# Performance work log

Hardware: AMD Instinct MI355X
Metric: run time of the kernel (lower is better)

## Reference

```python
import jax, jax.numpy as jnp
import numpy as np

DIM = 1024
HEADS = 16
HEAD_DIM = DIM // HEADS
B, S = 4, 2048


def setup_inputs() -> dict:
    key = jax.random.key(0)
    ks = jax.random.split(key, 10)
    std = 1.0 / np.sqrt(DIM)
    def lin(k):
        kw, kb = jax.random.split(k)
        W = jax.random.uniform(kw, (DIM, DIM), jnp.float32, -std, std)
        b = jax.random.uniform(kb, (DIM,), jnp.float32, -std, std)
        return W, b
    Wq, bq = lin(ks[0])
    Wk, bk = lin(ks[1])
    Wv, bv = lin(ks[2])
    Wo, bo = lin(ks[3])
    q = jax.random.normal(ks[4], (B, S, DIM), jnp.float32)
    mask = jnp.ones((B, S), dtype=bool)
    return {"q": q, "mask": mask, "Wq": Wq, "bq": bq, "Wk": Wk, "bk": bk,
            "Wv": Wv, "bv": bv, "Wo": Wo, "bo": bo}


def reference(q, mask, Wq, bq, Wk, bk, Wv, bv, Wo, bo):
    # self-attention: k = v = q
    Bsz, Sq, D = q.shape
    scale = HEAD_DIM ** -0.5
    qh = (q @ Wq.T + bq).reshape(Bsz, Sq, HEADS, HEAD_DIM)
    kh = (q @ Wk.T + bk).reshape(Bsz, Sq, HEADS, HEAD_DIM)
    vh = (q @ Wv.T + bv).reshape(Bsz, Sq, HEADS, HEAD_DIM)
    # scores: [B, H, Sq, Sk]
    scores = jnp.einsum('bqhd,bkhd->bhqk', qh, kh) * scale
    neg_inf = jnp.finfo(scores.dtype).min
    # padding mask (batch, seq) -> broadcast over heads and query dim
    scores = jnp.where(mask[:, None, None, :], scores, neg_inf)
    # causal mask
    causal = jnp.triu(jnp.ones((Sq, Sq), dtype=bool), k=1)
    scores = jnp.where(causal[None, None], neg_inf, scores)
    attn = jax.nn.softmax(scores, axis=-1)
    out = jnp.einsum('bhqk,bkhd->bqhd', attn, vh).reshape(Bsz, Sq, D)
    return out @ Wo.T + bo
```

## Files before the change

### kernel.cpp

```cpp
#include <hip/hip_runtime.h>
#include <stdint.h>

#define DIM   1024
#define HEADS 16
#define HD    64
#define BATCH 4
#define SEQ   2048
#define MTOT  (BATCH*SEQ)

typedef __attribute__((ext_vector_type(8))) short bf16x8;
typedef __attribute__((ext_vector_type(4))) float f32x4;

__device__ __forceinline__ unsigned short f2bf(float x) {
    unsigned int u = __float_as_uint(x);
    unsigned int r = (u + 0x7fffu + ((u >> 16) & 1u)) >> 16;
    return (unsigned short)r;
}

__device__ __forceinline__ unsigned int pkbf(float lo, float hi) {
    return __builtin_amdgcn_perm(__float_as_uint(hi) + 0x8000u,
                                 __float_as_uint(lo) + 0x8000u, 0x07060302u);
}
__device__ __forceinline__ unsigned int pktr(float lo, float hi) {
    return __builtin_amdgcn_perm(__float_as_uint(hi),
                                 __float_as_uint(lo), 0x07060302u);
}

__device__ __forceinline__ void gload_lds16(const void* g, void* l) {
    typedef __attribute__((address_space(1))) const unsigned int gbl_uint;
    typedef __attribute__((address_space(3))) unsigned int lds_uint;
    __builtin_amdgcn_global_load_lds(
        reinterpret_cast<gbl_uint*>(reinterpret_cast<uintptr_t>(g)),
        reinterpret_cast<lds_uint*>((unsigned int)reinterpret_cast<uintptr_t>(l)),
        16, 0, 0);
}

__global__ __launch_bounds__(256)
void cast_all(const float* __restrict__ q,
              const float* __restrict__ w0, const float* __restrict__ w1,
              const float* __restrict__ w2, const float* __restrict__ w3,
              unsigned short* __restrict__ qb, unsigned short* __restrict__ wb)
{
    size_t e = ((size_t)blockIdx.x * 256 + threadIdx.x) * 4;
    const float* src; unsigned short* dst; size_t off;
    if (e < (size_t)MTOT * DIM) { src = q; dst = qb; off = e; }
    else {
        size_t we = e - (size_t)MTOT * DIM;
        int wi = (int)(we >> 20);
        off = we & 1048575u;
        src = wi == 0 ? w0 : wi == 1 ? w1 : wi == 2 ? w2 : w3;
        dst = wb + (size_t)wi * 1048576;
    }
    float4 v = *(const float4*)(src + off);
    uint2 r; r.x = pkbf(v.x, v.y); r.y = pkbf(v.z, v.w);
    *(uint2*)(dst + off) = r;
}

template<bool OUT_F32>
__global__ __launch_bounds__(256)
void gemm_mfma(const unsigned short* __restrict__ X,
               const unsigned short* __restrict__ W0, const float* __restrict__ b0, void* __restrict__ O0,
               const unsigned short* __restrict__ W1, const float* __restrict__ b1, void* __restrict__ O1,
               const unsigned short* __restrict__ W2, const float* __restrict__ b2, void* __restrict__ O2,
               float scale0, int vt2)
{
    const unsigned short* W; const float* bias; void* Out;
    if (blockIdx.z == 0)      { W = W0; bias = b0; Out = O0; }
    else if (blockIdx.z == 1) { W = W1; bias = b1; Out = O1; }
    else                      { W = W2; bias = b2; Out = O2; }

    __shared__ unsigned short As[128 * 32];
    __shared__ unsigned short Bs[128 * 32];

    const int t    = threadIdx.x;
    const int wave = t >> 6;
    const int lane = t & 63;
    const int quad = lane >> 4;
    const int l16  = lane & 15;
    const int wm   = wave >> 1;
    const int wn   = wave & 1;
    const int m0   = blockIdx.y * 128;
    const int n0   = blockIdx.x * 128;

    const int srow = lane >> 2;
    const int skof = (lane & 3) * 8;

    f32x4 acc[4][4];
    #pragma unroll
    for (int i = 0; i < 4; ++i)
        #pragma unroll
        for (int j = 0; j < 4; ++j) acc[i][j] = (f32x4){0.f,0.f,0.f,0.f};

    for (int k0 = 0; k0 < 1024; k0 += 32) {
        __syncthreads();
        #pragma unroll
        for (int s = 0; s < 2; ++s) {
            const int ch = wave + s * 4;
            const int row = ch * 16 + srow;
            gload_lds16(X + (size_t)(m0 + row) * 1024 + k0 + skof, &As[ch * 512]);
            gload_lds16(W + (size_t)(n0 + row) * 1024 + k0 + skof, &Bs[ch * 512]);
        }
        __syncthreads();

        bf16x8 af[4], bfr[4];
        #pragma unroll
        for (int i = 0; i < 4; ++i)
            af[i] = *(const bf16x8*)&As[(wm * 64 + i * 16 + l16) * 32 + quad * 8];
        #pragma unroll
        for (int j = 0; j < 4; ++j)
            bfr[j] = *(const bf16x8*)&Bs[(wn * 64 + j * 16 + l16) * 32 + quad * 8];
        #pragma unroll
        for (int i = 0; i < 4; ++i)
            #pragma unroll
            for (int j = 0; j < 4; ++j)
                acc[i][j] = __builtin_amdgcn_mfma_f32_16x16x32_bf16(af[i], bfr[j], acc[i][j], 0, 0, 0);
    }

    const float sc = (blockIdx.z == 0) ? scale0 : 1.0f;
    const bool trans = (!OUT_F32) && vt2 && (blockIdx.z == 2);

    #pragma unroll
    for (int j = 0; j < 4; ++j) {
        const int col = n0 + wn * 64 + j * 16 + l16;
        const float bv = bias[col];
        #pragma unroll
        for (int i = 0; i < 4; ++i) {
            const int rowg = m0 + wm * 64 + i * 16 + quad * 4;
            if (trans) {
                const int bb = rowg >> 11, ss = rowg & 2047;
                const int hh = col >> 6, dd = col & 63;
                uint2 pk;
                pk.x = pkbf(acc[i][j][0] + bv, acc[i][j][1] + bv);
                pk.y = pkbf(acc[i][j][2] + bv, acc[i][j][3] + bv);
                *(uint2*)((unsigned short*)Out + ((size_t)((bb * 16 + hh) * 64 + dd)) * SEQ + ss) = pk;
            } else {
                #pragma unroll
                for (int r = 0; r < 4; ++r) {
                    float v = (acc[i][j][r] + bv) * sc;
                    if (OUT_F32)
                        ((float*)Out)[(size_t)(rowg + r) * 1024 + col] = v;
                    else
                        ((unsigned short*)Out)[(size_t)(rowg + r) * 1024 + col] = f2bf(v);
                }
            }
        }
    }
}

struct Job { int qt, kt0, kt1, part; };
__device__ const Job g_jobs[24] = {
    {15,0,16,0},{15,16,32,1},{7,0,16,2},
    {14,0,15,0},{14,15,30,1},
    {13,0,14,0},{13,14,28,1},{6,0,14,2},
    {12,0,13,0},{12,13,26,1},
    {11,0,12,0},{11,12,24,1},{5,0,12,2},
    {10,0,11,0},{10,11,22,1},
    {9,0,10,0},{9,10,20,1},{4,0,10,2},
    {8,0,9,0},{8,9,18,1},
    {3,0,8,2},{2,0,6,2},{1,0,4,2},{0,0,2,2},
};
#define PSTRIDE ((size_t)64*8*128)

__global__ __launch_bounds__(256)
void attn_mfma(const unsigned short* __restrict__ Qh,
               const unsigned short* __restrict__ Kh,
               const unsigned short* __restrict__ Vtg,
               unsigned short* __restrict__ Oh,
               float* __restrict__ Opart,
               float* __restrict__ Ml)
{
    __shared__ unsigned short Ks[64 * 72];
    __shared__ unsigned short Vs[64 * 72];
    __shared__ unsigned short Ps[128 * 72];

    const int t    = threadIdx.x;
    const int w    = t >> 6;
    const int lane = t & 63;
    const int quad = lane >> 4;
    const int l16  = lane & 15;

    const Job job = g_jobs[blockIdx.y];
    const int qt  = job.qt;
    const int bh  = blockIdx.x;
    const int b   = bh >> 4;
    const int h   = bh & 15;
    const int q0  = qt * 128;
    const size_t base  = (size_t)b * SEQ * DIM + (size_t)h * HD;
    const size_t vbase = (size_t)bh * HD * SEQ;

    bf16x8 onesf;
    #pragma unroll
    for (int e = 0; e < 8; ++e) onesf[e] = (short)0x3f80;

    bf16x8 qf[2][2];
    #pragma unroll
    for (int st = 0; st < 2; ++st) {
        const unsigned short* qp = Qh + base + (size_t)(q0 + (w * 2 + st) * 16 + l16) * DIM;
        qf[st][0] = *(const bf16x8*)(qp + quad * 8);
        qf[st][1] = *(const bf16x8*)(qp + 32 + quad * 8);
    }

    f32x4 oacc[2][4];
    f32x4 lacc[2];
    #pragma unroll
    for (int st = 0; st < 2; ++st) {
        lacc[st] = (f32x4){0.f,0.f,0.f,0.f};
        #pragma unroll
        for (int dj = 0; dj < 4; ++dj) oacc[st][dj] = (f32x4){0.f,0.f,0.f,0.f};
    }

    const int lrow = t >> 2;
    const int lcol = (t & 3) * 16;
    const unsigned short* kg = Kh + base + (size_t)lrow * DIM + lcol;
    const unsigned short* vg = Vtg + vbase + (size_t)lrow * SEQ + lcol;
    unsigned short* ksw = &Ks[lrow * 72 + lcol];
    unsigned short* vsw = &Vs[lrow * 72 + lcol];

    bf16x8 krg0, krg1, vrg0, vrg1;
    {
        const int k0p = job.kt0 * 64;
        krg0 = *(const bf16x8*)(kg + (size_t)k0p * DIM);
        krg1 = *(const bf16x8*)(kg + (size_t)k0p * DIM + 8);
        vrg0 = *(const bf16x8*)(vg + k0p);
        vrg1 = *(const bf16x8*)(vg + k0p + 8);
    }

    for (int kt = job.kt0; kt < job.kt1; ++kt) {
        const int k0 = kt * 64;
        __syncthreads();
        *(bf16x8*)ksw       = krg0;
        *(bf16x8*)(ksw + 8) = krg1;
        *(bf16x8*)vsw       = vrg0;
        *(bf16x8*)(vsw + 8) = vrg1;
        if (kt + 1 < job.kt1) {
            const int kn = k0 + 64;
            krg0 = *(const bf16x8*)(kg + (size_t)kn * DIM);
            krg1 = *(const bf16x8*)(kg + (size_t)kn * DIM + 8);
            vrg0 = *(const bf16x8*)(vg + kn);
            vrg1 = *(const bf16x8*)(vg + kn + 8);
        }
        __syncthreads();

        if (k0 > q0 + w * 32 + 31) continue;

        f32x4 scr[2][4];
        #pragma unroll
        for (int j = 0; j < 4; ++j) {
            bf16x8 kf0 = *(const bf16x8*)&Ks[(j * 16 + l16) * 72 + quad * 8];
            bf16x8 kf1 = *(const bf16x8*)&Ks[(j * 16 + l16) * 72 + 32 + quad * 8];
            #pragma unroll
            for (int st = 0; st < 2; ++st) {
                f32x4 acc0 = __builtin_amdgcn_mfma_f32_16x16x32_bf16(kf0, qf[st][0], (f32x4){0.f,0.f,0.f,0.f}, 0, 0, 0);
                scr[st][j] = __builtin_amdgcn_mfma_f32_16x16x32_bf16(kf1, qf[st][1], acc0, 0, 0, 0);
            }
        }

        #pragma unroll
        for (int st = 0; st < 2; ++st) {
            const int qs = (w * 2 + st) * 16;
            if (k0 + 63 > q0 + qs) {
                const int koff = k0 - q0 - qs + quad * 4;
                #pragma unroll
                for (int j = 0; j < 4; ++j)
                    #pragma unroll
                    for (int r = 0; r < 4; ++r)
                        if (j * 16 + koff + r > l16) scr[st][j][r] = -1e30f;
            }
            const int prow = (qs + l16) * 72;
            #pragma unroll
            for (int j = 0; j < 4; ++j) {
                float p0 = exp2f(scr[st][j][0]);
                float p1 = exp2f(scr[st][j][1]);
                float p2 = exp2f(scr[st][j][2]);
                float p3 = exp2f(scr[st][j][3]);
                uint2 pk; pk.x = pktr(p0, p1); pk.y = pktr(p2, p3);
                *(uint2*)&Ps[prow + j * 16 + quad * 4] = pk;
            }
        }

        bf16x8 pf[2][2];
        #pragma unroll
        for (int st = 0; st < 2; ++st) {
            const int prow = ((w * 2 + st) * 16 + l16) * 72;
            pf[st][0] = *(const bf16x8*)&Ps[prow + quad * 8];
            pf[st][1] = *(const bf16x8*)&Ps[prow + 32 + quad * 8];
        }
        #pragma unroll
        for (int dj = 0; dj < 4; ++dj) {
            bf16x8 vf0 = *(const bf16x8*)&Vs[(dj * 16 + l16) * 72 + quad * 8];
            bf16x8 vf1 = *(const bf16x8*)&Vs[(dj * 16 + l16) * 72 + 32 + quad * 8];
            #pragma unroll
            for (int st = 0; st < 2; ++st) {
                oacc[st][dj] = __builtin_amdgcn_mfma_f32_16x16x32_bf16(vf0, pf[st][0], oacc[st][dj], 0, 0, 0);
                oacc[st][dj] = __builtin_amdgcn_mfma_f32_16x16x32_bf16(vf1, pf[st][1], oacc[st][dj], 0, 0, 0);
            }
        }
        #pragma unroll
        for (int st = 0; st < 2; ++st) {
            lacc[st] = __builtin_amdgcn_mfma_f32_16x16x32_bf16(onesf, pf[st][0], lacc[st], 0, 0, 0);
            lacc[st] = __builtin_amdgcn_mfma_f32_16x16x32_bf16(onesf, pf[st][1], lacc[st], 0, 0, 0);
        }
    }

    if (job.part == 2) {
        #pragma unroll
        for (int st = 0; st < 2; ++st) {
            const float inv = 1.f / lacc[st][0];
            const size_t orow = base + (size_t)(q0 + (w * 2 + st) * 16 + l16) * DIM;
            #pragma unroll
            for (int dj = 0; dj < 4; ++dj) {
                uint2 pk;
                pk.x = pkbf(oacc[st][dj][0] * inv, oacc[st][dj][1] * inv);
                pk.y = pkbf(oacc[st][dj][2] * inv, oacc[st][dj][3] * inv);
                *(uint2*)&Oh[orow + dj * 16 + quad * 4] = pk;
            }
        }
    } else {
        const size_t jb = ((size_t)job.part * 64 + bh) * 8 + (qt - 8);
        #pragma unroll
        for (int st = 0; st < 2; ++st) {
            const int rl = (w * 2 + st) * 16 + l16;
            float* op = Opart + (jb * 128 + rl) * 64;
            #pragma unroll
            for (int dj = 0; dj < 4; ++dj) {
                float4 v;
                v.x = oacc[st][dj][0]; v.y = oacc[st][dj][1];
                v.z = oacc[st][dj][2]; v.w = oacc[st][dj][3];
                *(float4*)(op + dj * 16 + quad * 4) = v;
            }
            if (quad == 0) Ml[jb * 128 + rl] = lacc[st][0];
        }
    }
}

__global__ __launch_bounds__(256)
void attn_combine(const float* __restrict__ Opart, const float* __restrict__ Ml,
                  unsigned short* __restrict__ Oh)
{
    const int idx = blockIdx.x * 256 + threadIdx.x;
    const int d  = idx & 63;
    const int r  = (idx >> 6) & 127;
    const int qi = (idx >> 13) & 7;
    const int bh = idx >> 16;
    const size_t rbase = ((size_t)bh * 8 + qi) * 128 + r;
    const float l0 = Ml[rbase], l1 = Ml[PSTRIDE + rbase];
    const float o = (Opart[rbase * 64 + d] + Opart[(PSTRIDE + rbase) * 64 + d]) / (l0 + l1);
    const int b = bh >> 4, h = bh & 15;
    const int qq = (qi + 8) * 128 + r;
    Oh[(size_t)b * SEQ * DIM + (size_t)qq * DIM + h * 64 + d] = f2bf(o);
}

extern "C" void kernel_launch(void* const* d_in, const int* in_sizes, int n_in,
                              void* d_out, int out_size, void* d_ws, size_t ws_size,
                              hipStream_t stream)
{
    const float* q  = (const float*)d_in[0];
    const float* Wq = (const float*)d_in[2];
    const float* bq = (const float*)d_in[3];
    const float* Wk = (const float*)d_in[4];
    const float* bk = (const float*)d_in[5];
    const float* Wv = (const float*)d_in[6];
    const float* bv = (const float*)d_in[7];
    const float* Wo = (const float*)d_in[8];
    const float* bo = (const float*)d_in[9];

    unsigned short* qb  = (unsigned short*)d_ws;
    unsigned short* Wqb = qb  + (size_t)MTOT * DIM;
    unsigned short* Wkb = Wqb + (size_t)DIM * DIM;
    unsigned short* Wvb = Wkb + (size_t)DIM * DIM;
    unsigned short* Wob = Wvb + (size_t)DIM * DIM;
    unsigned short* qh  = Wob + (size_t)DIM * DIM;
    unsigned short* kh  = qh  + (size_t)MTOT * DIM;
    unsigned short* vt  = kh  + (size_t)MTOT * DIM;
    unsigned short* ao  = vt  + (size_t)MTOT * DIM;
    float* Opart = (float*)(ao + (size_t)MTOT * DIM);
    float* Ml    = Opart + 2 * PSTRIDE * 64;

    dim3 blk(256);

    hipLaunchKernelGGL(cast_all, dim3((MTOT * DIM + 4 * DIM * DIM) / 1024), blk, 0, stream,
                       q, Wq, Wk, Wv, Wo, qb, Wqb);

    dim3 g1(DIM / 128, MTOT / 128, 3);
    hipLaunchKernelGGL((gemm_mfma<false>), g1, blk, 0, stream,
                       qb, Wqb, bq, (void*)qh, Wkb, bk, (void*)kh, Wvb, bv, (void*)vt,
                       0.125f * 1.44269504089f, 1);

    dim3 g2(BATCH * HEADS, 24);
    hipLaunchKernelGGL(attn_mfma, g2, blk, 0, stream, qh, kh, vt, ao, Opart, Ml);

    hipLaunchKernelGGL(attn_combine, dim3((64 * 8 * 128 * 64) / 256), blk, 0, stream,
                       Opart, Ml, ao);

    dim3 g3(DIM / 128, MTOT / 128, 1);
    hipLaunchKernelGGL((gemm_mfma<true>), g3, blk, 0, stream,
                       ao, Wob, bo, d_out, Wob, bo, d_out, Wob, bo, d_out,
                       1.0f, 0);
}
```

Before: 290.6 us.

## Rebalance causal attention split-K jobs into finer chunks with bf16 partials

```diff
diff --git a/kernel.cpp b/kernel.cpp
--- a/kernel.cpp
+++ b/kernel.cpp
@@ -147,26 +147,26 @@
     }
 }
 
-struct Job { int qt, kt0, kt1, part; };
-__device__ const Job g_jobs[24] = {
-    {15,0,16,0},{15,16,32,1},{7,0,16,2},
-    {14,0,15,0},{14,15,30,1},
-    {13,0,14,0},{13,14,28,1},{6,0,14,2},
-    {12,0,13,0},{12,13,26,1},
-    {11,0,12,0},{11,12,24,1},{5,0,12,2},
-    {10,0,11,0},{10,11,22,1},
-    {9,0,10,0},{9,10,20,1},{4,0,10,2},
-    {8,0,9,0},{8,9,18,1},
-    {3,0,8,2},{2,0,6,2},{1,0,4,2},{0,0,2,2},
+struct Job { int qt, kt0, kt1, slot; };
+__device__ const Job g_jobs[40] = {
+    {3,0,8,-1},{7,0,8,6},{7,8,16,7},{10,0,8,14},
+    {11,0,8,17},{11,8,16,18},{11,16,24,19},{14,0,8,28},{14,8,16,29},
+    {15,0,8,32},{15,8,16,33},{15,16,24,34},{15,24,32,35},
+    {6,0,7,4},{6,7,14,5},{9,0,7,11},{9,7,14,12},{10,8,15,15},{10,15,22,16},
+    {12,0,7,20},{12,7,14,21},{13,0,7,24},{13,7,14,25},{13,14,21,26},{13,21,28,27},
+    {14,16,23,30},{14,23,30,31},
+    {2,0,6,-1},{5,0,6,2},{5,6,12,3},{8,0,6,8},{8,6,12,9},{8,12,18,10},
+    {9,14,20,13},{12,14,20,22},{12,20,26,23},
+    {4,0,5,0},{4,5,10,1},{1,0,4,-1},{0,0,2,-1},
 };
-#define PSTRIDE ((size_t)64*8*128)
+#define NSLOT 36
 
 __global__ __launch_bounds__(256)
 void attn_mfma(const unsigned short* __restrict__ Qh,
                const unsigned short* __restrict__ Kh,
                const unsigned short* __restrict__ Vtg,
                unsigned short* __restrict__ Oh,
-               float* __restrict__ Opart,
+               unsigned short* __restrict__ Opart,
                float* __restrict__ Ml)
 {
     __shared__ unsigned short Ks[64 * 72];
@@ -269,10 +269,10 @@
             const int prow = (qs + l16) * 72;
             #pragma unroll
             for (int j = 0; j < 4; ++j) {
-                float p0 = exp2f(scr[st][j][0]);
-                float p1 = exp2f(scr[st][j][1]);
-                float p2 = exp2f(scr[st][j][2]);
-                float p3 = exp2f(scr[st][j][3]);
+                float p0 = __builtin_amdgcn_exp2f(scr[st][j][0]);
+                float p1 = __builtin_amdgcn_exp2f(scr[st][j][1]);
+                float p2 = __builtin_amdgcn_exp2f(scr[st][j][2]);
+                float p3 = __builtin_amdgcn_exp2f(scr[st][j][3]);
                 uint2 pk; pk.x = pktr(p0, p1); pk.y = pktr(p2, p3);
                 *(uint2*)&Ps[prow + j * 16 + quad * 4] = pk;
             }
@@ -302,10 +302,10 @@
         }
     }
 
-    if (job.part == 2) {
+    if (job.slot < 0) {
         #pragma unroll
         for (int st = 0; st < 2; ++st) {
-            const float inv = 1.f / lacc[st][0];
+            const float inv = __builtin_amdgcn_rcpf(lacc[st][0]);
             const size_t orow = base + (size_t)(q0 + (w * 2 + st) * 16 + l16) * DIM;
             #pragma unroll
             for (int dj = 0; dj < 4; ++dj) {
@@ -316,38 +316,56 @@
             }
         }
     } else {
-        const size_t jb = ((size_t)job.part * 64 + bh) * 8 + (qt - 8);
+        const size_t sb = ((size_t)bh * NSLOT + job.slot) * 128;
         #pragma unroll
         for (int st = 0; st < 2; ++st) {
             const int rl = (w * 2 + st) * 16 + l16;
-            float* op = Opart + (jb * 128 + rl) * 64;
+            unsigned short* op = Opart + (sb + rl) * 64;
             #pragma unroll
             for (int dj = 0; dj < 4; ++dj) {
-                float4 v;
-                v.x = oacc[st][dj][0]; v.y = oacc[st][dj][1];
-                v.z = oacc[st][dj][2]; v.w = oacc[st][dj][3];
-                *(float4*)(op + dj * 16 + quad * 4) = v;
-            }
-            if (quad == 0) Ml[jb * 128 + rl] = lacc[st][0];
-        }
-    }
-}
+                uint2 pk;
+                pk.x = pkbf(oacc[st][dj][0], oacc[st][dj][1]);
+                pk.y = pkbf(oacc[st][dj][2], oacc[st][dj][3]);
+                *(uint2*)(op + dj * 16 + quad * 4) = pk;
+            }
+            if (quad == 0) Ml[sb + rl] = lacc[st][0];
+        }
+    }
+}
+
+__device__ const int c_slotBase[12] = {0,2,4,6,8,11,14,17,20,24,28,32};
+__device__ const int c_nparts[12]  = {2,2,2,2,3,3,3,3,4,4,4,4};
 
 __global__ __launch_bounds__(256)
-void attn_combine(const float* __restrict__ Opart, const float* __restrict__ Ml,
+void attn_combine(const unsigned short* __restrict__ Opart, const float* __restrict__ Ml,
                   unsigned short* __restrict__ Oh)
 {
     const int idx = blockIdx.x * 256 + threadIdx.x;
-    const int d  = idx & 63;
-    const int r  = (idx >> 6) & 127;
-    const int qi = (idx >> 13) & 7;
-    const int bh = idx >> 16;
-    const size_t rbase = ((size_t)bh * 8 + qi) * 128 + r;
-    const float l0 = Ml[rbase], l1 = Ml[PSTRIDE + rbase];
-    const float o = (Opart[rbase * 64 + d] + Opart[(PSTRIDE + rbase) * 64 + d]) / (l0 + l1);
+    const int d4  = idx & 15;
+    const int r   = (idx >> 4) & 127;
+    const int rest = idx >> 11;
+    const int qti = rest % 12;
+    const int bh  = rest / 12;
+    const int np  = c_nparts[qti];
+    const size_t sb = (size_t)bh * NSLOT + c_slotBase[qti];
+
+    float o0 = 0.f, o1 = 0.f, o2 = 0.f, o3 = 0.f, l = 0.f;
+    for (int p = 0; p < np; ++p) {
+        const size_t rb = (sb + p) * 128 + r;
+        uint2 pk = *(const uint2*)(Opart + rb * 64 + d4 * 4);
+        o0 += __uint_as_float(pk.x << 16);
+        o1 += __uint_as_float(pk.x & 0xffff0000u);
+        o2 += __uint_as_float(pk.y << 16);
+        o3 += __uint_as_float(pk.y & 0xffff0000u);
+        l  += Ml[rb];
+    }
+    const float inv = __builtin_amdgcn_rcpf(l);
     const int b = bh >> 4, h = bh & 15;
-    const int qq = (qi + 8) * 128 + r;
-    Oh[(size_t)b * SEQ * DIM + (size_t)qq * DIM + h * 64 + d] = f2bf(o);
+    const int qq = (qti + 4) * 128 + r;
+    uint2 outp;
+    outp.x = pkbf(o0 * inv, o1 * inv);
+    outp.y = pkbf(o2 * inv, o3 * inv);
+    *(uint2*)&Oh[(size_t)b * SEQ * DIM + (size_t)qq * DIM + h * 64 + d4 * 4] = outp;
 }
 
 extern "C" void kernel_launch(void* const* d_in, const int* in_sizes, int n_in,
@@ -373,8 +391,8 @@
     unsigned short* kh  = qh  + (size_t)MTOT * DIM;
     unsigned short* vt  = kh  + (size_t)MTOT * DIM;
     unsigned short* ao  = vt  + (size_t)MTOT * DIM;
-    float* Opart = (float*)(ao + (size_t)MTOT * DIM);
-    float* Ml    = Opart + 2 * PSTRIDE * 64;
+    unsigned short* Opart = ao + (size_t)MTOT * DIM;
+    float* Ml = (float*)qb;
 
     dim3 blk(256);
 
@@ -386,10 +404,10 @@
                        qb, Wqb, bq, (void*)qh, Wkb, bk, (void*)kh, Wvb, bv, (void*)vt,
                        0.125f * 1.44269504089f, 1);
 
-    dim3 g2(BATCH * HEADS, 24);
+    dim3 g2(BATCH * HEADS, 40);
     hipLaunchKernelGGL(attn_mfma, g2, blk, 0, stream, qh, kh, vt, ao, Opart, Ml);
 
-    hipLaunchKernelGGL(attn_combine, dim3((64 * 8 * 128 * 64) / 256), blk, 0, stream,
+    hipLaunchKernelGGL(attn_combine, dim3((64 * 12 * 128 * 16) / 256), blk, 0, stream,
                        Opart, Ml, ao);
 
     dim3 g3(DIM / 128, MTOT / 128, 1);
```

Result: faster. 280.4 us (-3.5%).
